# Performance work log

Hardware: AMD Instinct MI355X
Metric: run time of the kernel (lower is better)

The kernel has to match this reference:

```python
import jax, jax.numpy as jnp
import numpy as np

B, H, W, C = 2, 64, 64, 512
EPS = 1e-3  # keras BatchNormalization default epsilon


def _bn(x, g, b, m, v):
    # inference-mode batch norm over the last axis
    return (x - m) * jax.lax.rsqrt(v + EPS) * g + b


def setup_inputs() -> dict:
    key = jax.random.key(0)
    ks = jax.random.split(key, 12)
    C2 = C // 2

    def he(k, shape, fan_in):
        return jax.random.normal(k, shape, jnp.float32) * np.float32(np.sqrt(2.0 / fan_in))

    def bn_params(k, n):
        k1, k2, k3, k4 = jax.random.split(k, 4)
        g = 1.0 + 0.1 * jax.random.normal(k1, (n,), jnp.float32)
        b = 0.1 * jax.random.normal(k2, (n,), jnp.float32)
        m = 0.1 * jax.random.normal(k3, (n,), jnp.float32)
        v = jax.random.uniform(k4, (n,), jnp.float32, 0.5, 1.5)
        return g, b, m, v

    g1, b1, m1, v1 = bn_params(ks[1], 1)
    g2, b2, m2, v2 = bn_params(ks[2], C2)
    g3, b3, m3, v3 = bn_params(ks[3], C2)
    g4, b4, m4, v4 = bn_params(ks[4], 1)
    g5, b5, m5, v5 = bn_params(ks[5], C)

    return {
        "x": jax.random.normal(ks[0], (B, H, W, C), jnp.float32),
        # edge_aggregation_func: Dense(1) over the 4-neighbor axis
        "w_ea": he(ks[6], (4, 1), 4), "b_ea": jnp.zeros((1,), jnp.float32),
        "g1": g1, "b1": b1, "m1": m1, "v1": v1,
        # vertex_update_func: Dense(C//2) over 2C features
        "w_vu": he(ks[7], (2 * C, C2), 2 * C), "b_vu": jnp.zeros((C2,), jnp.float32),
        "g2": g2, "b2": b2, "m2": m2, "v2": v2,
        # edge_update_func: Dense(C//2) over 2C features
        "w_eu": he(ks[8], (2 * C, C2), 2 * C), "b_eu": jnp.zeros((C2,), jnp.float32),
        "g3": g3, "b3": b3, "m3": m3, "v3": v3,
        # update_edge_reduce_func: Dense(1) over the 4-neighbor axis
        "w_er": he(ks[9], (4, 1), 4), "b_er": jnp.zeros((1,), jnp.float32),
        "g4": g4, "b4": b4, "m4": m4, "v4": v4,
        # final 1x1 conv (no bias): [C + C//2, C]
        "w_fc": he(ks[10], (C + C2, C), C + C2),
        "g5": g5, "b5": b5, "m5": m5, "v5": v5,
    }


def reference(x, w_ea, b_ea, g1, b1, m1, v1,
              w_vu, b_vu, g2, b2, m2, v2,
              w_eu, b_eu, g3, b3, m3, v3,
              w_er, b_er, g4, b4, m4, v4,
              w_fc, g5, b5, m5, v5):
    # 4-neighbor cyclic-shift edges: [B,H,W,C,4] (H+1, H-1, W+1, W-1 rolls)
    neigh = jnp.stack([
        jnp.roll(x, 1, axis=1), jnp.roll(x, -1, axis=1),
        jnp.roll(x, 1, axis=2), jnp.roll(x, -1, axis=2)], axis=-1)
    edge = neigh * x[..., None]                                   # [B,H,W,C,4]

    # edge aggregation: Dense(1) over neighbor axis + BN(1) + ReLU
    agg = jax.nn.relu(_bn(jnp.einsum('bhwcn,no->bhwco', edge, w_ea) + b_ea,
                          g1, b1, m1, v1))[..., 0]                # [B,H,W,C]

    # vertex update: Dense(C/2) on concat([vertex, agg]) + BN + ReLU
    cat_v = jnp.concatenate([x, agg], axis=-1)                    # [B,H,W,2C]
    uv = jax.nn.relu(_bn(cat_v @ w_vu + b_vu, g2, b2, m2, v2))    # [B,H,W,C/2]

    # edge update: Dense(C/2) on concat([vertex x4, edge]) along channel
    vert4 = jnp.broadcast_to(x[..., None], edge.shape)            # [B,H,W,C,4]
    cat_e = jnp.concatenate([vert4, edge], axis=3)                # [B,H,W,2C,4]
    ue = jax.nn.relu(_bn(jnp.einsum('bhwcn,cd->bhwnd', cat_e, w_eu) + b_eu,
                         g3, b3, m3, v3))                          # [B,H,W,4,C/2]

    # reduce updated edges over neighbor axis: Dense(1) + BN(1) + ReLU
    ur = jax.nn.relu(_bn(jnp.einsum('bhwnd,no->bhwdo', ue, w_er) + b_er,
                         g4, b4, m4, v4))[..., 0]                 # [B,H,W,C/2]

    update_feature = uv * ur                                      # [B,H,W,C/2]

    # final aggregation: 1x1 conv (no bias) on concat([x, update]) + BN + ReLU
    out = jax.nn.relu(_bn(jnp.concatenate([x, update_feature], axis=-1) @ w_fc,
                          g5, b5, m5, v5))                         # [B,H,W,C]
    return out
```

## Files before the change

kernel.cpp:

```cpp
#include <hip/hip_runtime.h>
#include <stdint.h>


typedef __attribute__((ext_vector_type(8))) short bf16x8;
typedef __attribute__((ext_vector_type(4))) float f32x4;

#define EPS_BN 1e-3f

__device__ __forceinline__ short f2bf(float f) {
    union { float f; unsigned u; } cv;
    cv.f = f;
    unsigned r = cv.u + 0x7fffu + ((cv.u >> 16) & 1u);
    return (short)(r >> 16);
}
__device__ __forceinline__ float bf2f(short s) {
    union { unsigned u; float f; } cv;
    cv.u = ((unsigned)(unsigned short)s) << 16;
    return cv.f;
}


__device__ __forceinline__ void pack_one(const float* __restrict__ W, short* __restrict__ out,
                                         int K, int Ncol, int lb, int tid) {
    int i = lb * 256 + tid;
    int lane = i & 63, tile = i >> 6;
    int ktiles = K >> 5;
    int nt = tile / ktiles, kt = tile - nt * ktiles;
    int kbase = (kt << 5) + ((lane >> 4) << 3);
    int col = (nt << 4) + (lane & 15);
    bf16x8 v;
    #pragma unroll
    for (int j = 0; j < 8; ++j) v[j] = f2bf(W[(kbase + j) * Ncol + col]);
    ((bf16x8*)out)[(tile << 6) + lane] = v;
}

__global__ __launch_bounds__(256) void k_front(
    const float* __restrict__ x,
    const float* w_ea, const float* b_ea,
    const float* g1, const float* b1, const float* m1, const float* v1,
    const float* w_vu, const float* w_eu, const float* w_fc,
    const float* b_vu, const float* g2, const float* b2_, const float* m2, const float* v2,
    const float* b_eu, const float* g3, const float* b3, const float* m3, const float* v3,
    const float* w_er, const float* b_er,
    const float* g4, const float* b4, const float* m4, const float* v4,
    const float* g5, const float* b5, const float* m5, const float* v5,
    short* __restrict__ xb, short* __restrict__ agg,
    short* BpVu, short* BpEu, short* BpFc, float* P)
{
    int blk = blockIdx.x, t = threadIdx.x;
    if (blk >= 2048) {
        int b = blk - 2048;
        if (b < 128)      { pack_one(w_vu, BpVu, 1024, 256, b, t); }
        else if (b < 256) { pack_one(w_eu, BpEu, 1024, 256, b - 128, t); }
        else if (b < 448) { pack_one(w_fc, BpFc,  768, 512, b - 256, t); }
        else {
            for (int u = t; u < 512; u += 256) {
                float a5 = g5[u] * rsqrtf(v5[u] + EPS_BN);
                P[1032 + u] = a5;
                P[1544 + u] = b5[u] - m5[u] * a5;
            }
            {
                float a2 = g2[t] * rsqrtf(v2[t] + EPS_BN);
                P[8 + t]   = a2;
                P[264 + t] = (b_vu[t] - m2[t]) * a2 + b2_[t];
                float a3 = g3[t] * rsqrtf(v3[t] + EPS_BN);
                P[520 + t] = a3;
                P[776 + t] = (b_eu[t] - m3[t]) * a3 + b3[t];
            }
            if (t < 4) {
                P[2056 + t] = w_ea[t];
                P[2060 + t] = w_er[t];
            }
            if (t == 0) {
                float a4 = g4[0] * rsqrtf(v4[0] + EPS_BN);
                P[2] = a4;
                P[3] = (b_er[0] - m4[0]) * a4 + b4[0];
                float a1l = g1[0] * rsqrtf(v1[0] + EPS_BN);
                P[0] = a1l;
                P[1] = (b_ea[0] - m1[0]) * a1l + b1[0];
            }
        }
        return;
    }

    float a1 = g1[0] * rsqrtf(v1[0] + EPS_BN);
    float c1 = (b_ea[0] - m1[0]) * a1 + b1[0];
    float w0 = w_ea[0], w1 = w_ea[1], w2 = w_ea[2], w3 = w_ea[3];

    int idx = blk * 256 + t;
    int n = idx >> 6;
    int ci = idx & 63;
    int bh = n >> 6, h = bh & 63, w = n & 63;
    int bhb = bh & ~63;
    int rowU = ((bhb + ((h + 63) & 63)) << 6) + w;
    int rowD = ((bhb + ((h + 1) & 63)) << 6) + w;
    int rowL = (bh << 6) + ((w + 63) & 63);
    int rowR = (bh << 6) + ((w + 1) & 63);

    const f32x4* xv = (const f32x4*)x;
    int c4 = ci << 1;
    f32x4 vc[2], vU[2], vD[2], vL[2], vR[2];
    #pragma unroll
    for (int h2 = 0; h2 < 2; ++h2) {
        vc[h2] = xv[(n    << 7) + c4 + h2];
        vU[h2] = xv[(rowU << 7) + c4 + h2];
        vD[h2] = xv[(rowD << 7) + c4 + h2];
        vL[h2] = xv[(rowL << 7) + c4 + h2];
        vR[h2] = xv[(rowR << 7) + c4 + h2];
    }

    bf16x8 ob, xbv;
    #pragma unroll
    for (int h2 = 0; h2 < 2; ++h2) {
        #pragma unroll
        for (int j = 0; j < 4; ++j) {
            int e = h2 * 4 + j;
            float xc = vc[h2][j];
            float S = w0 * (xc * vU[h2][j]) + w1 * (xc * vD[h2][j])
                    + w2 * (xc * vL[h2][j]) + w3 * (xc * vR[h2][j]);
            ob[e]  = f2bf(fmaxf(fmaf(a1, S, c1), 0.f));
            xbv[e] = f2bf(xc);
        }
    }
    int o = (n << 6) + ci;
    ((bf16x8*)agg)[o] = ob;
    ((bf16x8*)xb)[o] = xbv;
}

#define MID_LOAD(ga, na_, kc) do {                                            \
    const short* _S; int _off;                                                \
    if (type == 0) { _S = ((kc) < 8) ? xb : agg; _off = ((kc) & 7) << 6; }    \
    else           { _S = xb; _off = (kc) << 6; }                             \
    ga = *(const bf16x8*)(_S + sAoff + _off + lcs);                           \
    if (type >= 2) na_ = *(const bf16x8*)(xb + nAoff + _off + lcs);           \
} while (0)

#define MID_WRITE(slot, ga, na_) do {                                         \
    bf16x8 _va = ga;                                                          \
    if (type >= 2) {                                                          \
        _Pragma("unroll") for (int _j = 0; _j < 8; ++_j)                      \
            _va[_j] = f2bf(bf2f(_va[_j]) * bf2f(na_[_j]));                    \
    }                                                                         \
    ((bf16x8*)sA[slot])[t] = _va;                                             \
} while (0)

#define MID_COMPUTE(slot, kc) do {                                            \
    const short* _Lb = sA[slot];                                              \
    _Pragma("unroll") for (int _kt = 0; _kt < 2; ++_kt) {                     \
        bf16x8 _af[2];                                                        \
        _Pragma("unroll") for (int _mi = 0; _mi < 2; ++_mi) {                 \
            int _row = (_mi << 4) + (l & 15);                                 \
            int _lcolb = (_kt << 6) + ((l >> 4) << 4);                        \
            int _addr = (_row << 6) + ((_lcolb ^ ((_row & 7) << 4)) >> 1);    \
            _af[_mi] = *(const bf16x8*)(_Lb + _addr);                         \
        }                                                                     \
        int _kt32 = ktbase + ((kc) << 1) + _kt;                               \
        _Pragma("unroll") for (int _nf = 0; _nf < 4; ++_nf) {                 \
            bf16x8 _b = Bp[((((w << 2) + _nf) << 5) + _kt32) * 64 + l];       \
            _Pragma("unroll") for (int _mi = 0; _mi < 2; ++_mi)               \
                acc[_mi][_nf] = __builtin_amdgcn_mfma_f32_16x16x32_bf16(      \
                    _af[_mi], _b, acc[_mi][_nf], 0, 0, 0);                    \
        }                                                                     \
    }                                                                         \
} while (0)

__global__ __launch_bounds__(256) void k_gemm_mid(
    const short* __restrict__ xb, const short* __restrict__ agg,
    const short* __restrict__ BpVu, const short* __restrict__ BpEu,
    const float* __restrict__ P,
    short* __restrict__ uvb, short* __restrict__ tvb,
    short* __restrict__ teDb, short* __restrict__ teRb)
{
    __shared__ __align__(16) short sA[2][32 * 64];
    int t = threadIdx.x, l = t & 63, w = t >> 6;
    int type = blockIdx.x >> 8, rs = blockIdx.x & 255;
    int r0 = rs << 5;
    int dr = t >> 3, p8 = t & 7;
    int lcs = (p8 ^ (dr & 7)) << 3;

    int rA = r0 + dr;
    int nA = rA;
    if (type == 2) {
        int bh = rA >> 6;
        nA = (((bh & ~63) + (((bh & 63) + 1) & 63)) << 6) + (rA & 63);
    } else if (type == 3) {
        nA = (rA & ~63) + ((rA + 1) & 63);
    }
    int sAoff = rA << 9, nAoff = nA << 9;

    int nchunk = (type == 0) ? 16 : 8;
    const bf16x8* Bp = (type == 0) ? (const bf16x8*)BpVu : (const bf16x8*)BpEu;
    int ktbase = (type >= 2) ? 16 : 0;
    short* Out = (type == 0) ? uvb : (type == 1) ? tvb : (type == 2) ? teDb : teRb;

    f32x4 acc[2][4];
    #pragma unroll
    for (int mi = 0; mi < 2; ++mi)
        #pragma unroll
        for (int nf = 0; nf < 4; ++nf) acc[mi][nf] = (f32x4){0.f, 0.f, 0.f, 0.f};

    bf16x8 gA, nAv, gB, nBv;
    MID_LOAD(gA, nAv, 0);
    MID_LOAD(gB, nBv, 1);

    for (int kc2 = 0; kc2 < nchunk; kc2 += 2) {
        MID_WRITE(0, gA, nAv);
        __syncthreads();
        if (kc2 + 2 < nchunk) MID_LOAD(gA, nAv, kc2 + 2);
        MID_COMPUTE(0, kc2);
        MID_WRITE(1, gB, nBv);
        __syncthreads();
        if (kc2 + 3 < nchunk) MID_LOAD(gB, nBv, kc2 + 3);
        MID_COMPUTE(1, kc2 + 1);
    }

    #pragma unroll
    for (int nf = 0; nf < 4; ++nf) {
        int col = (w << 6) + (nf << 4) + (l & 15);
        float aa = P[8 + col], cc = P[264 + col];
        #pragma unroll
        for (int mi = 0; mi < 2; ++mi) {
            int rbase = r0 + (mi << 4) + ((l >> 4) << 2);
            #pragma unroll
            for (int j = 0; j < 4; ++j) {
                float v = acc[mi][nf][j];
                if (type == 0) v = fmaxf(fmaf(v, aa, cc), 0.f);
                Out[(rbase + j) * 256 + col] = f2bf(v);
            }
        }
    }
}

#define OUT_COMPUTE(Lb, kc) do {                                              \
    _Pragma("unroll") for (int _kt = 0; _kt < 2; ++_kt) {                     \
        bf16x8 _af[2];                                                        \
        _Pragma("unroll") for (int _mi = 0; _mi < 2; ++_mi) {                 \
            int _row = (_mi << 4) + (l & 15);                                 \
            int _lcolb = (_kt << 6) + ((l >> 4) << 4);                        \
            int _addr = (_row << 6) + ((_lcolb ^ ((_row & 7) << 4)) >> 1);    \
            _af[_mi] = *(const bf16x8*)((Lb) + _addr);                        \
        }                                                                     \
        _Pragma("unroll") for (int _nf = 0; _nf < 2; ++_nf) {                 \
            int _nt = (cq << 3) + (w << 1) + _nf;                             \
            bf16x8 _b = Bp[(_nt * 24 + ((kc) << 1) + _kt) * 64 + l];          \
            _Pragma("unroll") for (int _mi = 0; _mi < 2; ++_mi)               \
                acc[_mi][_nf] = __builtin_amdgcn_mfma_f32_16x16x32_bf16(      \
                    _af[_mi], _b, acc[_mi][_nf], 0, 0, 0);                    \
        }                                                                     \
    }                                                                         \
} while (0)

__global__ __launch_bounds__(256) void k_gemm_out(
    const short* __restrict__ xb,
    const short* __restrict__ tv, const short* __restrict__ teD,
    const short* __restrict__ teR, const short* __restrict__ uv,
    const short* __restrict__ BpFc, const float* __restrict__ P,
    float* __restrict__ out)
{
    __shared__ __align__(16) short sXb[2][32 * 64];
    __shared__ __align__(16) short updL[4][32 * 64];
    int t = threadIdx.x, l = t & 63, w = t >> 6;
    int cq = blockIdx.x & 3, rs = blockIdx.x >> 2;
    int r0 = rs << 5;
    const bf16x8* Bp = (const bf16x8*)BpFc;

    int dr = t >> 3, p8 = t & 7;
    int lcs = (p8 ^ (dr & 7)) << 3;
    int xrow = (r0 + dr) << 9;

    bf16x8 gA = *(const bf16x8*)(xb + xrow + lcs);
    bf16x8 gB = *(const bf16x8*)(xb + xrow + 64 + lcs);

    {
        int n = r0 + dr;
        int bh = n >> 6, h = bh & 63, ww = n & 63;
        int bhb = bh & ~63;
        int nUp = ((bhb + ((h + 63) & 63)) << 6) + ww;
        int nLf = (bh << 6) + ((ww + 63) & 63);
        float w0 = P[2060], w1 = P[2061], w2 = P[2062], w3 = P[2063];
        float a4 = P[2], c4 = P[3];
        #pragma unroll
        for (int q = 0; q < 4; ++q) {
            int lc = (q << 6) + lcs;
            bf16x8 vTv = *(const bf16x8*)(tv  + n   * 256 + lc);
            bf16x8 vD  = *(const bf16x8*)(teD + n   * 256 + lc);
            bf16x8 vDu = *(const bf16x8*)(teD + nUp * 256 + lc);
            bf16x8 vR  = *(const bf16x8*)(teR + n   * 256 + lc);
            bf16x8 vRl = *(const bf16x8*)(teR + nLf * 256 + lc);
            bf16x8 vUv = *(const bf16x8*)(uv  + n   * 256 + lc);
            f32x4 a3a = *(const f32x4*)&P[520 + lc], a3b = *(const f32x4*)&P[524 + lc];
            f32x4 c3a = *(const f32x4*)&P[776 + lc], c3b = *(const f32x4*)&P[780 + lc];
            bf16x8 o;
            #pragma unroll
            for (int j = 0; j < 8; ++j) {
                float a3 = (j < 4) ? a3a[j & 3] : a3b[j & 3];
                float c3 = (j < 4) ? c3a[j & 3] : c3b[j & 3];
                float tvv = bf2f(vTv[j]);
                float ueU = fmaxf(fmaf(a3, tvv + bf2f(vDu[j]), c3), 0.f);
                float ueD = fmaxf(fmaf(a3, tvv + bf2f(vD[j]),  c3), 0.f);
                float ueL = fmaxf(fmaf(a3, tvv + bf2f(vRl[j]), c3), 0.f);
                float ueR = fmaxf(fmaf(a3, tvv + bf2f(vR[j]),  c3), 0.f);
                float s = w0 * ueU + w1 * ueD + w2 * ueL + w3 * ueR;
                float ur = fmaxf(fmaf(a4, s, c4), 0.f);
                o[j] = f2bf(ur * bf2f(vUv[j]));
            }
            *(bf16x8*)&updL[q][(dr << 6) + (p8 << 3)] = o;
        }
    }

    f32x4 acc[2][2];
    #pragma unroll
    for (int mi = 0; mi < 2; ++mi)
        #pragma unroll
        for (int nf = 0; nf < 2; ++nf) acc[mi][nf] = (f32x4){0.f, 0.f, 0.f, 0.f};

    for (int kc2 = 0; kc2 < 8; kc2 += 2) {
        ((bf16x8*)sXb[0])[t] = gA;
        __syncthreads();
        if (kc2 + 2 < 8) gA = *(const bf16x8*)(xb + xrow + ((kc2 + 2) << 6) + lcs);
        OUT_COMPUTE(sXb[0], kc2);
        ((bf16x8*)sXb[1])[t] = gB;
        __syncthreads();
        if (kc2 + 3 < 8) gB = *(const bf16x8*)(xb + xrow + ((kc2 + 3) << 6) + lcs);
        OUT_COMPUTE(sXb[1], kc2 + 1);
    }
    #pragma unroll
    for (int ku = 0; ku < 4; ++ku) OUT_COMPUTE(updL[ku], 8 + ku);

    #pragma unroll
    for (int nf = 0; nf < 2; ++nf) {
        int col = (cq << 7) + (w << 5) + (nf << 4) + (l & 15);
        float a5 = P[1032 + col], c5 = P[1544 + col];
        #pragma unroll
        for (int mi = 0; mi < 2; ++mi) {
            int rbase = r0 + (mi << 4) + ((l >> 4) << 2);
            #pragma unroll
            for (int j = 0; j < 4; ++j) {
                out[(rbase + j) * 512 + col] = fmaxf(fmaf(acc[mi][nf][j], a5, c5), 0.f);
            }
        }
    }
}

extern "C" void kernel_launch(void* const* d_in, const int* in_sizes, int n_in,
                              void* d_out, int out_size, void* d_ws, size_t ws_size,
                              hipStream_t stream)
{
    const float* x    = (const float*)d_in[0];
    const float* w_ea = (const float*)d_in[1];
    const float* b_ea = (const float*)d_in[2];
    const float* g1   = (const float*)d_in[3];
    const float* b1   = (const float*)d_in[4];
    const float* m1   = (const float*)d_in[5];
    const float* v1   = (const float*)d_in[6];
    const float* w_vu = (const float*)d_in[7];
    const float* b_vu = (const float*)d_in[8];
    const float* g2   = (const float*)d_in[9];
    const float* b2   = (const float*)d_in[10];
    const float* m2   = (const float*)d_in[11];
    const float* v2   = (const float*)d_in[12];
    const float* w_eu = (const float*)d_in[13];
    const float* b_eu = (const float*)d_in[14];
    const float* g3   = (const float*)d_in[15];
    const float* b3   = (const float*)d_in[16];
    const float* m3   = (const float*)d_in[17];
    const float* v3   = (const float*)d_in[18];
    const float* w_er = (const float*)d_in[19];
    const float* b_er = (const float*)d_in[20];
    const float* g4   = (const float*)d_in[21];
    const float* b4   = (const float*)d_in[22];
    const float* m4   = (const float*)d_in[23];
    const float* v4   = (const float*)d_in[24];
    const float* w_fc = (const float*)d_in[25];
    const float* g5   = (const float*)d_in[26];
    const float* b5   = (const float*)d_in[27];
    const float* m5   = (const float*)d_in[28];
    const float* v5   = (const float*)d_in[29];

    char* ws = (char*)d_ws;
    float* P = (float*)ws;
    size_t off = 16384;
    short* BpVu = (short*)(ws + off); off += (size_t)1024 * 256 * 2;
    short* BpEu = (short*)(ws + off); off += (size_t)1024 * 256 * 2;
    short* BpFc = (short*)(ws + off); off += (size_t)768 * 512 * 2;
    short* xbb  = (short*)(ws + off); off += (size_t)8192 * 512 * 2;
    short* aggb = (short*)(ws + off); off += (size_t)8192 * 512 * 2;
    short* uvb  = (short*)(ws + off); off += (size_t)8192 * 256 * 2;
    short* tvb  = (short*)(ws + off); off += (size_t)8192 * 256 * 2;
    short* teDb = (short*)(ws + off); off += (size_t)8192 * 256 * 2;
    short* teRb = (short*)(ws + off); off += (size_t)8192 * 256 * 2;

    k_front<<<2497, 256, 0, stream>>>(x, w_ea, b_ea, g1, b1, m1, v1,
                                      w_vu, w_eu, w_fc,
                                      b_vu, g2, b2, m2, v2,
                                      b_eu, g3, b3, m3, v3,
                                      w_er, b_er, g4, b4, m4, v4,
                                      g5, b5, m5, v5,
                                      xbb, aggb, BpVu, BpEu, BpFc, P);
    k_gemm_mid<<<1024, 256, 0, stream>>>(xbb, aggb, BpVu, BpEu, P,
                                         uvb, tvb, teDb, teRb);
    k_gemm_out<<<1024, 256, 0, stream>>>(xbb, tvb, teDb, teRb, uvb, BpFc, P,
                                         (float*)d_out);
}
```

Before: 65.62 us.

## Fuse three edge-update GEMM types into one block sharing the vertex tile loads

The mid GEMM kernel previously launched separate block types for the vertex term and the two shifted-neighbor edge terms, each reloading the vertex rows. Now one block loads the vertex tile once, forms both neighbor products, and runs three MFMA accumulator sets over a half-width column slice, while the vertex-update GEMM keeps its own blocks. This cuts redundant global loads of xb and the grid from 1024 to 768 blocks. In exchange it triples LDS use and accumulator registers per block, which may lower occupancy.

```diff
diff --git a/kernel.cpp b/kernel.cpp
--- a/kernel.cpp
+++ b/kernel.cpp
@@ -127,25 +127,59 @@
     ((bf16x8*)xb)[o] = xbv;
 }
 
-#define MID_LOAD(ga, na_, kc) do {                                            \
-    const short* _S; int _off;                                                \
-    if (type == 0) { _S = ((kc) < 8) ? xb : agg; _off = ((kc) & 7) << 6; }    \
-    else           { _S = xb; _off = (kc) << 6; }                             \
-    ga = *(const bf16x8*)(_S + sAoff + _off + lcs);                           \
-    if (type >= 2) na_ = *(const bf16x8*)(xb + nAoff + _off + lcs);           \
+
+#define E_LOAD(gx, gd, gr, kc) do {                                           \
+    gx = *(const bf16x8*)(xb + xoff + ((kc) << 6) + lcs);                     \
+    gd = *(const bf16x8*)(xb + doff + ((kc) << 6) + lcs);                     \
+    gr = *(const bf16x8*)(xb + roff + ((kc) << 6) + lcs);                     \
 } while (0)
 
-#define MID_WRITE(slot, ga, na_) do {                                         \
-    bf16x8 _va = ga;                                                          \
-    if (type >= 2) {                                                          \
-        _Pragma("unroll") for (int _j = 0; _j < 8; ++_j)                      \
-            _va[_j] = f2bf(bf2f(_va[_j]) * bf2f(na_[_j]));                    \
+#define E_WRITE(slot, gx, gd, gr) do {                                        \
+    bf16x8 _vd, _vr;                                                          \
+    _Pragma("unroll") for (int _j = 0; _j < 8; ++_j) {                        \
+        float _x = bf2f(gx[_j]);                                              \
+        _vd[_j] = f2bf(_x * bf2f(gd[_j]));                                    \
+        _vr[_j] = f2bf(_x * bf2f(gr[_j]));                                    \
     }                                                                         \
-    ((bf16x8*)sA[slot])[t] = _va;                                             \
+    ((bf16x8*)sX[slot])[t] = gx;                                              \
+    ((bf16x8*)sD[slot])[t] = _vd;                                             \
+    ((bf16x8*)sR[slot])[t] = _vr;                                             \
 } while (0)
 
-#define MID_COMPUTE(slot, kc) do {                                            \
-    const short* _Lb = sA[slot];                                              \
+#define E_COMPUTE(slot, kc) do {                                              \
+    const short* _LX = sX[slot];                                              \
+    const short* _LD = sD[slot];                                              \
+    const short* _LR = sR[slot];                                              \
+    _Pragma("unroll") for (int _kt = 0; _kt < 2; ++_kt) {                     \
+        bf16x8 _aX[2], _aD[2], _aR[2];                                        \
+        _Pragma("unroll") for (int _mi = 0; _mi < 2; ++_mi) {                 \
+            int _row = (_mi << 4) + (l & 15);                                 \
+            int _lcolb = (_kt << 6) + ((l >> 4) << 4);                        \
+            int _addr = (_row << 6) + ((_lcolb ^ ((_row & 7) << 4)) >> 1);    \
+            _aX[_mi] = *(const bf16x8*)(_LX + _addr);                         \
+            _aD[_mi] = *(const bf16x8*)(_LD + _addr);                         \
+            _aR[_mi] = *(const bf16x8*)(_LR + _addr);                         \
+        }                                                                     \
+        int _kt32 = ((kc) << 1) + _kt;                                        \
+        _Pragma("unroll") for (int _nf = 0; _nf < 2; ++_nf) {                 \
+            bf16x8 _bT = Be[((nt0 + _nf) * 32 + _kt32) * 64 + l];             \
+            bf16x8 _bB = Be[((nt0 + _nf) * 32 + 16 + _kt32) * 64 + l];        \
+            _Pragma("unroll") for (int _mi = 0; _mi < 2; ++_mi) {             \
+                aV[_mi][_nf] = __builtin_amdgcn_mfma_f32_16x16x32_bf16(       \
+                    _aX[_mi], _bT, aV[_mi][_nf], 0, 0, 0);                    \
+                aD_[_mi][_nf] = __builtin_amdgcn_mfma_f32_16x16x32_bf16(      \
+                    _aD[_mi], _bB, aD_[_mi][_nf], 0, 0, 0);                   \
+                aR_[_mi][_nf] = __builtin_amdgcn_mfma_f32_16x16x32_bf16(      \
+                    _aR[_mi], _bB, aR_[_mi][_nf], 0, 0, 0);                   \
+            }                                                                 \
+        }                                                                     \
+    }                                                                         \
+} while (0)
+
+#define UV_SRC(kc) (((kc) < 8 ? xb : agg) + xoff + (((kc) & 7) << 6) + lcs)
+
+#define UV_COMPUTE(slot, kc) do {                                             \
+    const short* _Lb = sX[slot];                                              \
     _Pragma("unroll") for (int _kt = 0; _kt < 2; ++_kt) {                     \
         bf16x8 _af[2];                                                        \
         _Pragma("unroll") for (int _mi = 0; _mi < 2; ++_mi) {                 \
@@ -154,9 +188,9 @@
             int _addr = (_row << 6) + ((_lcolb ^ ((_row & 7) << 4)) >> 1);    \
             _af[_mi] = *(const bf16x8*)(_Lb + _addr);                         \
         }                                                                     \
-        int _kt32 = ktbase + ((kc) << 1) + _kt;                               \
+        int _kt32 = ((kc) << 1) + _kt;                                        \
         _Pragma("unroll") for (int _nf = 0; _nf < 4; ++_nf) {                 \
-            bf16x8 _b = Bp[((((w << 2) + _nf) << 5) + _kt32) * 64 + l];       \
+            bf16x8 _b = Bv[((((w << 2) + _nf) << 5) + _kt32) * 64 + l];       \
             _Pragma("unroll") for (int _mi = 0; _mi < 2; ++_mi)               \
                 acc[_mi][_nf] = __builtin_amdgcn_mfma_f32_16x16x32_bf16(      \
                     _af[_mi], _b, acc[_mi][_nf], 0, 0, 0);                    \
@@ -171,61 +205,100 @@
     short* __restrict__ uvb, short* __restrict__ tvb,
     short* __restrict__ teDb, short* __restrict__ teRb)
 {
-    __shared__ __align__(16) short sA[2][32 * 64];
+    __shared__ __align__(16) short sX[2][32 * 64];
+    __shared__ __align__(16) short sD[2][32 * 64];
+    __shared__ __align__(16) short sR[2][32 * 64];
     int t = threadIdx.x, l = t & 63, w = t >> 6;
-    int type = blockIdx.x >> 8, rs = blockIdx.x & 255;
-    int r0 = rs << 5;
+    int bid = blockIdx.x;
     int dr = t >> 3, p8 = t & 7;
     int lcs = (p8 ^ (dr & 7)) << 3;
 
-    int rA = r0 + dr;
-    int nA = rA;
-    if (type == 2) {
+    if (bid < 512) {
+        int rs = bid >> 1, ch = bid & 1;
+        int r0 = rs << 5;
+        int rA = r0 + dr;
         int bh = rA >> 6;
-        nA = (((bh & ~63) + (((bh & 63) + 1) & 63)) << 6) + (rA & 63);
-    } else if (type == 3) {
-        nA = (rA & ~63) + ((rA + 1) & 63);
-    }
-    int sAoff = rA << 9, nAoff = nA << 9;
-
-    int nchunk = (type == 0) ? 16 : 8;
-    const bf16x8* Bp = (type == 0) ? (const bf16x8*)BpVu : (const bf16x8*)BpEu;
-    int ktbase = (type >= 2) ? 16 : 0;
-    short* Out = (type == 0) ? uvb : (type == 1) ? tvb : (type == 2) ? teDb : teRb;
-
-    f32x4 acc[2][4];
-    #pragma unroll
-    for (int mi = 0; mi < 2; ++mi)
-        #pragma unroll
-        for (int nf = 0; nf < 4; ++nf) acc[mi][nf] = (f32x4){0.f, 0.f, 0.f, 0.f};
-
-    bf16x8 gA, nAv, gB, nBv;
-    MID_LOAD(gA, nAv, 0);
-    MID_LOAD(gB, nBv, 1);
-
-    for (int kc2 = 0; kc2 < nchunk; kc2 += 2) {
-        MID_WRITE(0, gA, nAv);
-        __syncthreads();
-        if (kc2 + 2 < nchunk) MID_LOAD(gA, nAv, kc2 + 2);
-        MID_COMPUTE(0, kc2);
-        MID_WRITE(1, gB, nBv);
-        __syncthreads();
-        if (kc2 + 3 < nchunk) MID_LOAD(gB, nBv, kc2 + 3);
-        MID_COMPUTE(1, kc2 + 1);
-    }
-
-    #pragma unroll
-    for (int nf = 0; nf < 4; ++nf) {
-        int col = (w << 6) + (nf << 4) + (l & 15);
-        float aa = P[8 + col], cc = P[264 + col];
-        #pragma unroll
-        for (int mi = 0; mi < 2; ++mi) {
-            int rbase = r0 + (mi << 4) + ((l >> 4) << 2);
-            #pragma unroll
-            for (int j = 0; j < 4; ++j) {
-                float v = acc[mi][nf][j];
-                if (type == 0) v = fmaxf(fmaf(v, aa, cc), 0.f);
-                Out[(rbase + j) * 256 + col] = f2bf(v);
+        int nD = (((bh & ~63) + (((bh & 63) + 1) & 63)) << 6) + (rA & 63);
+        int nR = (rA & ~63) + ((rA + 1) & 63);
+        int xoff = rA << 9, doff = nD << 9, roff = nR << 9;
+        int nt0 = (ch << 3) + (w << 1);
+        const bf16x8* Be = (const bf16x8*)BpEu;
+
+        f32x4 aV[2][2], aD_[2][2], aR_[2][2];
+        #pragma unroll
+        for (int mi = 0; mi < 2; ++mi)
+            #pragma unroll
+            for (int nf = 0; nf < 2; ++nf) {
+                aV[mi][nf]  = (f32x4){0.f, 0.f, 0.f, 0.f};
+                aD_[mi][nf] = (f32x4){0.f, 0.f, 0.f, 0.f};
+                aR_[mi][nf] = (f32x4){0.f, 0.f, 0.f, 0.f};
+            }
+
+        bf16x8 gX0, gD0, gR0, gX1, gD1, gR1;
+        E_LOAD(gX0, gD0, gR0, 0);
+        E_LOAD(gX1, gD1, gR1, 1);
+        for (int kc2 = 0; kc2 < 8; kc2 += 2) {
+            E_WRITE(0, gX0, gD0, gR0);
+            __syncthreads();
+            if (kc2 + 2 < 8) E_LOAD(gX0, gD0, gR0, kc2 + 2);
+            E_COMPUTE(0, kc2);
+            E_WRITE(1, gX1, gD1, gR1);
+            __syncthreads();
+            if (kc2 + 3 < 8) E_LOAD(gX1, gD1, gR1, kc2 + 3);
+            E_COMPUTE(1, kc2 + 1);
+        }
+
+        #pragma unroll
+        for (int nf = 0; nf < 2; ++nf) {
+            int col = (ch << 7) + (w << 5) + (nf << 4) + (l & 15);
+            #pragma unroll
+            for (int mi = 0; mi < 2; ++mi) {
+                int rbase = r0 + (mi << 4) + ((l >> 4) << 2);
+                #pragma unroll
+                for (int j = 0; j < 4; ++j) {
+                    tvb [(rbase + j) * 256 + col] = f2bf(aV[mi][nf][j]);
+                    teDb[(rbase + j) * 256 + col] = f2bf(aD_[mi][nf][j]);
+                    teRb[(rbase + j) * 256 + col] = f2bf(aR_[mi][nf][j]);
+                }
+            }
+        }
+    } else {
+        int rs = bid - 512;
+        int r0 = rs << 5;
+        int xoff = (r0 + dr) << 9;
+        const bf16x8* Bv = (const bf16x8*)BpVu;
+
+        f32x4 acc[2][4];
+        #pragma unroll
+        for (int mi = 0; mi < 2; ++mi)
+            #pragma unroll
+            for (int nf = 0; nf < 4; ++nf) acc[mi][nf] = (f32x4){0.f, 0.f, 0.f, 0.f};
+
+        bf16x8 gA = *(const bf16x8*)UV_SRC(0);
+        bf16x8 gB = *(const bf16x8*)UV_SRC(1);
+        for (int kc2 = 0; kc2 < 16; kc2 += 2) {
+            ((bf16x8*)sX[0])[t] = gA;
+            __syncthreads();
+            if (kc2 + 2 < 16) gA = *(const bf16x8*)UV_SRC(kc2 + 2);
+            UV_COMPUTE(0, kc2);
+            ((bf16x8*)sX[1])[t] = gB;
+            __syncthreads();
+            if (kc2 + 3 < 16) gB = *(const bf16x8*)UV_SRC(kc2 + 3);
+            UV_COMPUTE(1, kc2 + 1);
+        }
+
+        #pragma unroll
+        for (int nf = 0; nf < 4; ++nf) {
+            int col = (w << 6) + (nf << 4) + (l & 15);
+            float aa = P[8 + col], cc = P[264 + col];
+            #pragma unroll
+            for (int mi = 0; mi < 2; ++mi) {
+                int rbase = r0 + (mi << 4) + ((l >> 4) << 2);
+                #pragma unroll
+                for (int j = 0; j < 4; ++j) {
+                    float v = fmaxf(fmaf(acc[mi][nf][j], aa, cc), 0.f);
+                    uvb[(rbase + j) * 256 + col] = f2bf(v);
+                }
             }
         }
     }
@@ -397,8 +470,8 @@
                                       w_er, b_er, g4, b4, m4, v4,
                                       g5, b5, m5, v5,
                                       xbb, aggb, BpVu, BpEu, BpFc, P);
-    k_gemm_mid<<<1024, 256, 0, stream>>>(xbb, aggb, BpVu, BpEu, P,
-                                         uvb, tvb, teDb, teRb);
+    k_gemm_mid<<<768, 256, 0, stream>>>(xbb, aggb, BpVu, BpEu, P,
+                                        uvb, tvb, teDb, teRb);
     k_gemm_out<<<1024, 256, 0, stream>>>(xbb, tvb, teDb, teRb, uvb, BpFc, P,
                                          (float*)d_out);
 }
```

New measurement: 90.27 us. +37.6%, slower.

## Restructure mid GEMM to stage weights in LDS and precompute edge products

Applied to the files above, without the earlier changes.

The front kernel now also writes bf16 down and right edge products (x times the shifted neighbour), so the mid GEMM no longer forms these products on the fly. The mid kernel is reorganised: each block stages a 64-column slice of the packed weights into a 64 KB shared buffer and streams A fragments straight from global memory. One block computes the vertex-term GEMM together with both edge GEMMs, sharing the staged B. Grid size is halved. This trades extra global writes and reads for the product buffers, plus lower occupancy from the large LDS footprint, for more B reuse and fewer A staging passes.

```diff
diff --git a/kernel.cpp b/kernel.cpp
--- a/kernel.cpp
+++ b/kernel.cpp
@@ -45,6 +45,7 @@
     const float* g4, const float* b4, const float* m4, const float* v4,
     const float* g5, const float* b5, const float* m5, const float* v5,
     short* __restrict__ xb, short* __restrict__ agg,
+    short* __restrict__ prodD, short* __restrict__ prodR,
     short* BpVu, short* BpEu, short* BpFc, float* P)
 {
     int blk = blockIdx.x, t = threadIdx.x;
@@ -109,123 +110,153 @@
         vR[h2] = xv[(rowR << 7) + c4 + h2];
     }
 
-    bf16x8 ob, xbv;
+    bf16x8 ob, xbv, pD, pR;
     #pragma unroll
     for (int h2 = 0; h2 < 2; ++h2) {
         #pragma unroll
         for (int j = 0; j < 4; ++j) {
             int e = h2 * 4 + j;
             float xc = vc[h2][j];
-            float S = w0 * (xc * vU[h2][j]) + w1 * (xc * vD[h2][j])
-                    + w2 * (xc * vL[h2][j]) + w3 * (xc * vR[h2][j]);
+            float eU = xc * vU[h2][j], eD = xc * vD[h2][j];
+            float eL = xc * vL[h2][j], eR = xc * vR[h2][j];
+            float S = w0 * eU + w1 * eD + w2 * eL + w3 * eR;
             ob[e]  = f2bf(fmaxf(fmaf(a1, S, c1), 0.f));
             xbv[e] = f2bf(xc);
+            pD[e] = f2bf(eD);
+            pR[e] = f2bf(eR);
         }
     }
     int o = (n << 6) + ci;
     ((bf16x8*)agg)[o] = ob;
     ((bf16x8*)xb)[o] = xbv;
-}
-
-#define MID_LOAD(ga, na_, kc) do {                                            \
-    const short* _S; int _off;                                                \
-    if (type == 0) { _S = ((kc) < 8) ? xb : agg; _off = ((kc) & 7) << 6; }    \
-    else           { _S = xb; _off = (kc) << 6; }                             \
-    ga = *(const bf16x8*)(_S + sAoff + _off + lcs);                           \
-    if (type >= 2) na_ = *(const bf16x8*)(xb + nAoff + _off + lcs);           \
+    ((bf16x8*)prodD)[o] = pD;
+    ((bf16x8*)prodR)[o] = pR;
+}
+
+
+#define MFMA16(a, b, c) __builtin_amdgcn_mfma_f32_16x16x32_bf16(a, b, c, 0, 0, 0)
+
+#define STAGE_B(Bsrc, ktoff) do {                                             \
+    const bf16x8* _g = (const bf16x8*)(Bsrc);                                 \
+    bf16x8* _s = (bf16x8*)sB;                                                 \
+    _Pragma("unroll") for (int _i = 0; _i < 16; ++_i) {                       \
+        int _u = (_i << 8) + t;                                               \
+        int _ntl = _u >> 10;                                                  \
+        _s[_u] = _g[((cs4 + _ntl) << 11) + ((ktoff) << 6) + (_u & 1023)];     \
+    }                                                                         \
 } while (0)
 
-#define MID_WRITE(slot, ga, na_) do {                                         \
-    bf16x8 _va = ga;                                                          \
-    if (type >= 2) {                                                          \
-        _Pragma("unroll") for (int _j = 0; _j < 8; ++_j)                      \
-            _va[_j] = f2bf(bf2f(_va[_j]) * bf2f(na_[_j]));                    \
-    }                                                                         \
-    ((bf16x8*)sA[slot])[t] = _va;                                             \
-} while (0)
-
-#define MID_COMPUTE(slot, kc) do {                                            \
-    const short* _Lb = sA[slot];                                              \
-    _Pragma("unroll") for (int _kt = 0; _kt < 2; ++_kt) {                     \
-        bf16x8 _af[2];                                                        \
-        _Pragma("unroll") for (int _mi = 0; _mi < 2; ++_mi) {                 \
-            int _row = (_mi << 4) + (l & 15);                                 \
-            int _lcolb = (_kt << 6) + ((l >> 4) << 4);                        \
-            int _addr = (_row << 6) + ((_lcolb ^ ((_row & 7) << 4)) >> 1);    \
-            _af[_mi] = *(const bf16x8*)(_Lb + _addr);                         \
-        }                                                                     \
-        int _kt32 = ktbase + ((kc) << 1) + _kt;                               \
-        _Pragma("unroll") for (int _nf = 0; _nf < 4; ++_nf) {                 \
-            bf16x8 _b = Bp[((((w << 2) + _nf) << 5) + _kt32) * 64 + l];       \
-            _Pragma("unroll") for (int _mi = 0; _mi < 2; ++_mi)               \
-                acc[_mi][_nf] = __builtin_amdgcn_mfma_f32_16x16x32_bf16(      \
-                    _af[_mi], _b, acc[_mi][_nf], 0, 0, 0);                    \
+#define SWEEP1(S, acc) do {                                                   \
+    _Pragma("unroll") for (int _kt = 0; _kt < 16; ++_kt) {                    \
+        bf16x8 _a0 = *(const bf16x8*)((S) + ((arow0      ) << 9) + (_kt << 5) + kseg); \
+        bf16x8 _a1 = *(const bf16x8*)((S) + ((arow0 + 16 ) << 9) + (_kt << 5) + kseg); \
+        _Pragma("unroll") for (int _n = 0; _n < 4; ++_n) {                    \
+            bf16x8 _b = ((const bf16x8*)sB)[(_n << 10) + (_kt << 6) + l];     \
+            acc[0][_n] = MFMA16(_a0, _b, acc[0][_n]);                         \
+            acc[1][_n] = MFMA16(_a1, _b, acc[1][_n]);                         \
         }                                                                     \
     }                                                                         \
 } while (0)
 
+#define SWEEP2(S1, accD, S2, accR) do {                                       \
+    _Pragma("unroll") for (int _kt = 0; _kt < 16; ++_kt) {                    \
+        bf16x8 _d0 = *(const bf16x8*)((S1) + ((arow0      ) << 9) + (_kt << 5) + kseg); \
+        bf16x8 _d1 = *(const bf16x8*)((S1) + ((arow0 + 16 ) << 9) + (_kt << 5) + kseg); \
+        bf16x8 _r0 = *(const bf16x8*)((S2) + ((arow0      ) << 9) + (_kt << 5) + kseg); \
+        bf16x8 _r1 = *(const bf16x8*)((S2) + ((arow0 + 16 ) << 9) + (_kt << 5) + kseg); \
+        _Pragma("unroll") for (int _n = 0; _n < 4; ++_n) {                    \
+            bf16x8 _b = ((const bf16x8*)sB)[(_n << 10) + (_kt << 6) + l];     \
+            accD[0][_n] = MFMA16(_d0, _b, accD[0][_n]);                       \
+            accD[1][_n] = MFMA16(_d1, _b, accD[1][_n]);                       \
+            accR[0][_n] = MFMA16(_r0, _b, accR[0][_n]);                       \
+            accR[1][_n] = MFMA16(_r1, _b, accR[1][_n]);                       \
+        }                                                                     \
+    }                                                                         \
+} while (0)
+
+#define ZERO_ACC(acc)                                                         \
+    _Pragma("unroll") for (int _m = 0; _m < 2; ++_m)                          \
+        _Pragma("unroll") for (int _n = 0; _n < 4; ++_n)                      \
+            acc[_m][_n] = (f32x4){0.f, 0.f, 0.f, 0.f}
+
 __global__ __launch_bounds__(256) void k_gemm_mid(
     const short* __restrict__ xb, const short* __restrict__ agg,
+    const short* __restrict__ prodD, const short* __restrict__ prodR,
     const short* __restrict__ BpVu, const short* __restrict__ BpEu,
     const float* __restrict__ P,
     short* __restrict__ uvb, short* __restrict__ tvb,
     short* __restrict__ teDb, short* __restrict__ teRb)
 {
-    __shared__ __align__(16) short sA[2][32 * 64];
+    __shared__ __align__(16) short sB[64 * 512];
     int t = threadIdx.x, l = t & 63, w = t >> 6;
-    int type = blockIdx.x >> 8, rs = blockIdx.x & 255;
-    int r0 = rs << 5;
-    int dr = t >> 3, p8 = t & 7;
-    int lcs = (p8 ^ (dr & 7)) << 3;
-
-    int rA = r0 + dr;
-    int nA = rA;
-    if (type == 2) {
-        int bh = rA >> 6;
-        nA = (((bh & ~63) + (((bh & 63) + 1) & 63)) << 6) + (rA & 63);
-    } else if (type == 3) {
-        nA = (rA & ~63) + ((rA + 1) & 63);
-    }
-    int sAoff = rA << 9, nAoff = nA << 9;
-
-    int nchunk = (type == 0) ? 16 : 8;
-    const bf16x8* Bp = (type == 0) ? (const bf16x8*)BpVu : (const bf16x8*)BpEu;
-    int ktbase = (type >= 2) ? 16 : 0;
-    short* Out = (type == 0) ? uvb : (type == 1) ? tvb : (type == 2) ? teDb : teRb;
-
-    f32x4 acc[2][4];
-    #pragma unroll
-    for (int mi = 0; mi < 2; ++mi)
-        #pragma unroll
-        for (int nf = 0; nf < 4; ++nf) acc[mi][nf] = (f32x4){0.f, 0.f, 0.f, 0.f};
-
-    bf16x8 gA, nAv, gB, nBv;
-    MID_LOAD(gA, nAv, 0);
-    MID_LOAD(gB, nBv, 1);
-
-    for (int kc2 = 0; kc2 < nchunk; kc2 += 2) {
-        MID_WRITE(0, gA, nAv);
-        __syncthreads();
-        if (kc2 + 2 < nchunk) MID_LOAD(gA, nAv, kc2 + 2);
-        MID_COMPUTE(0, kc2);
-        MID_WRITE(1, gB, nBv);
-        __syncthreads();
-        if (kc2 + 3 < nchunk) MID_LOAD(gB, nBv, kc2 + 3);
-        MID_COMPUTE(1, kc2 + 1);
-    }
-
-    #pragma unroll
-    for (int nf = 0; nf < 4; ++nf) {
-        int col = (w << 6) + (nf << 4) + (l & 15);
-        float aa = P[8 + col], cc = P[264 + col];
-        #pragma unroll
-        for (int mi = 0; mi < 2; ++mi) {
-            int rbase = r0 + (mi << 4) + ((l >> 4) << 2);
+    int bid = blockIdx.x;
+    int sub = (bid < 256) ? bid : bid - 256;
+    int cs = sub & 3, rg = sub >> 2;
+    int r0 = rg << 7;
+    int rw = r0 + (w << 5);
+    int cs4 = cs << 2;
+    int arow0 = rw + (l & 15);
+    int kseg = (l >> 4) << 3;
+
+    if (bid < 256) {
+        f32x4 aV[2][4];
+        ZERO_ACC(aV);
+        STAGE_B(BpEu, 0);
+        __syncthreads();
+        SWEEP1(xb, aV);
+        #pragma unroll
+        for (int nn = 0; nn < 4; ++nn) {
+            int col = (cs << 6) + (nn << 4) + (l & 15);
             #pragma unroll
-            for (int j = 0; j < 4; ++j) {
-                float v = acc[mi][nf][j];
-                if (type == 0) v = fmaxf(fmaf(v, aa, cc), 0.f);
-                Out[(rbase + j) * 256 + col] = f2bf(v);
+            for (int mi = 0; mi < 2; ++mi) {
+                int rb = rw + (mi << 4) + ((l >> 4) << 2);
+                #pragma unroll
+                for (int j = 0; j < 4; ++j)
+                    tvb[(rb + j) * 256 + col] = f2bf(aV[mi][nn][j]);
+            }
+        }
+        __syncthreads();
+        STAGE_B(BpEu, 16);
+        __syncthreads();
+        f32x4 aD[2][4], aR[2][4];
+        ZERO_ACC(aD);
+        ZERO_ACC(aR);
+        SWEEP2(prodD, aD, prodR, aR);
+        #pragma unroll
+        for (int nn = 0; nn < 4; ++nn) {
+            int col = (cs << 6) + (nn << 4) + (l & 15);
+            #pragma unroll
+            for (int mi = 0; mi < 2; ++mi) {
+                int rb = rw + (mi << 4) + ((l >> 4) << 2);
+                #pragma unroll
+                for (int j = 0; j < 4; ++j) {
+                    teDb[(rb + j) * 256 + col] = f2bf(aD[mi][nn][j]);
+                    teRb[(rb + j) * 256 + col] = f2bf(aR[mi][nn][j]);
+                }
+            }
+        }
+    } else {
+        f32x4 acc[2][4];
+        ZERO_ACC(acc);
+        STAGE_B(BpVu, 0);
+        __syncthreads();
+        SWEEP1(xb, acc);
+        __syncthreads();
+        STAGE_B(BpVu, 16);
+        __syncthreads();
+        SWEEP1(agg, acc);
+        #pragma unroll
+        for (int nn = 0; nn < 4; ++nn) {
+            int col = (cs << 6) + (nn << 4) + (l & 15);
+            float aa = P[8 + col], cc = P[264 + col];
+            #pragma unroll
+            for (int mi = 0; mi < 2; ++mi) {
+                int rb = rw + (mi << 4) + ((l >> 4) << 2);
+                #pragma unroll
+                for (int j = 0; j < 4; ++j) {
+                    float v = fmaxf(fmaf(acc[mi][nn][j], aa, cc), 0.f);
+                    uvb[(rb + j) * 256 + col] = f2bf(v);
+                }
             }
         }
     }
@@ -385,6 +416,8 @@
     short* BpFc = (short*)(ws + off); off += (size_t)768 * 512 * 2;
     short* xbb  = (short*)(ws + off); off += (size_t)8192 * 512 * 2;
     short* aggb = (short*)(ws + off); off += (size_t)8192 * 512 * 2;
+    short* prodD = (short*)(ws + off); off += (size_t)8192 * 512 * 2;
+    short* prodR = (short*)(ws + off); off += (size_t)8192 * 512 * 2;
     short* uvb  = (short*)(ws + off); off += (size_t)8192 * 256 * 2;
     short* tvb  = (short*)(ws + off); off += (size_t)8192 * 256 * 2;
     short* teDb = (short*)(ws + off); off += (size_t)8192 * 256 * 2;
@@ -396,9 +429,11 @@
                                       b_eu, g3, b3, m3, v3,
                                       w_er, b_er, g4, b4, m4, v4,
                                       g5, b5, m5, v5,
-                                      xbb, aggb, BpVu, BpEu, BpFc, P);
-    k_gemm_mid<<<1024, 256, 0, stream>>>(xbb, aggb, BpVu, BpEu, P,
-                                         uvb, tvb, teDb, teRb);
+                                      xbb, aggb, prodD, prodR,
+                                      BpVu, BpEu, BpFc, P);
+    k_gemm_mid<<<512, 256, 0, stream>>>(xbb, aggb, prodD, prodR,
+                                        BpVu, BpEu, P,
+                                        uvb, tvb, teDb, teRb);
     k_gemm_out<<<1024, 256, 0, stream>>>(xbb, tvb, teDb, teRb, uvb, BpFc, P,
                                          (float*)d_out);
 }
```

Result: slower. 76.04 us (+15.9%).
